# Kernel optimization log

Hardware: AMD Instinct MI355X
Metric: run time of the kernel (lower is better)

## Reference

```python
import jax, jax.numpy as jnp
import numpy as np

H = 256      # hidden_dim
NH = 8       # num_heads
D = H // NH  # per-head dim
NEG = -(2.0**32) + 1.0
EPS = 1e-5


def setup_inputs() -> dict:
    key = jax.random.key(0)
    ks = jax.random.split(key, 12)
    N, Tq, Tk = 2, 2048, 2048
    s = 1.0 / np.sqrt(H)
    return {
        "Q": jax.random.normal(ks[0], (N, Tq, H), jnp.float32),
        "K": jax.random.normal(ks[1], (N, Tk, H), jnp.float32),
        "V": jax.random.normal(ks[2], (N, Tk, H), jnp.float32),
        "Wq": jax.random.normal(ks[3], (H, H), jnp.float32) * s,
        "bq": jnp.zeros((H,), jnp.float32),
        "Wk": jax.random.normal(ks[4], (H, H), jnp.float32) * s,
        "bk": jnp.zeros((H,), jnp.float32),
        "Wv": jax.random.normal(ks[5], (H, H), jnp.float32) * s,
        "bv": jnp.zeros((H,), jnp.float32),
        "gamma": jnp.ones((H,), jnp.float32),
        "beta": jnp.zeros((H,), jnp.float32),
    }


def _split_heads(x):
    # [N,T,H] -> [h,N,T,D]  (matches torch split(dim=2)+cat(dim=0): head-major)
    N, T, _ = x.shape
    return x.reshape(N, T, NH, D).transpose(2, 0, 1, 3)


def reference(Q, K, V, Wq, bq, Wk, bk, Wv, bv, gamma, beta):
    N, Tq, _ = Q.shape
    Tk = K.shape[1]
    Ql = jax.nn.relu(Q @ Wq + bq)
    Kl = jax.nn.relu(K @ Wk + bk)
    Vl = jax.nn.relu(V @ Wv + bv)
    Qh, Kh, Vh = _split_heads(Ql), _split_heads(Kl), _split_heads(Vl)

    scores = jnp.einsum("hnqd,hnkd->hnqk", Qh, Kh) / jnp.sqrt(jnp.float32(D))
    key_mask = jnp.sign(jnp.abs(K).sum(-1))    # [N,Tk]
    scores = jnp.where(key_mask[None, :, None, :] == 0, NEG, scores)
    attn = jax.nn.softmax(scores / 0.01, axis=-1)
    query_mask = jnp.sign(jnp.abs(Q).sum(-1))  # [N,Tq]
    attn = attn * query_mask[None, :, :, None]  # dropout p=0 -> identity

    ctx = jnp.einsum("hnqk,hnkd->hnqd", attn[..., :-1], Vh[:, :, :-1, :])
    out = ctx.transpose(1, 2, 0, 3).reshape(N, Tq, H)

    mu = out.mean(-1, keepdims=True)
    var = ((out - mu) ** 2).mean(-1, keepdims=True)
    out = (out - mu) / jnp.sqrt(var + EPS) * gamma + beta

    weight = attn.transpose(1, 2, 0, 3).reshape(N, Tq, NH * Tk).mean(-1)
    return out, weight
```

## Files before the change

### kernel.cpp

```cpp
#include <hip/hip_runtime.h>
#include <math.h>

#define H_DIM 256
#define NHEAD 8
#define DHEAD 32
#define NB 2
#define TSEQ 2048
#define LN_EPS 1e-5f

#define QK2_SCALE 25.503486f
#define NEG2 (-6.2e11f)
#define SPLIT 4
#define TILES_PER (TSEQ / 64 / SPLIT)

typedef _Float16 half8 __attribute__((ext_vector_type(8)));
typedef float f32x4 __attribute__((ext_vector_type(4)));

__device__ __forceinline__ f32x4 mfma16(half8 a, half8 b, f32x4 c) {
  return __builtin_amdgcn_mfma_f32_16x16x32_f16(a, b, c, 0, 0, 0);
}
__device__ __forceinline__ float exp2fast(float x) {
  return __builtin_amdgcn_exp2f(x);
}
#define DPP_MAX4(mx, CTRL)                                                   \
  {                                                                          \
    _Pragma("unroll")                                                        \
    for (int r = 0; r < 4; ++r) {                                            \
      int t_ = __builtin_amdgcn_update_dpp(0, __float_as_int(mx[r]), CTRL,   \
                                           0xf, 0xf, false);                 \
      mx[r] = fmaxf(mx[r], __int_as_float(t_));                              \
    }                                                                        \
  }

__global__ __launch_bounds__(256) void mask_kernel(
    const float* __restrict__ Q, const float* __restrict__ K,
    float* __restrict__ qmask, float* __restrict__ kmask) {
  const int wid = threadIdx.x >> 6, lane = threadIdx.x & 63;
  int row = blockIdx.x * 4 + wid;
  const int total_q = NB * TSEQ;
  const float* src;
  float* dst;
  if (row < total_q) { src = Q + (size_t)row * H_DIM; dst = qmask + row; }
  else               { src = K + (size_t)(row - total_q) * H_DIM; dst = kmask + (row - total_q); }
  float4 v = *(const float4*)(src + lane * 4);
  float s = fabsf(v.x) + fabsf(v.y) + fabsf(v.z) + fabsf(v.w);
  #pragma unroll
  for (int off = 32; off > 0; off >>= 1) s += __shfl_xor(s, off);
  if (lane == 0) *dst = (s != 0.0f) ? 1.0f : 0.0f;
}

__global__ __launch_bounds__(256) void prepack_kernel(
    const float* __restrict__ Wq, const float* __restrict__ Wk, const float* __restrict__ Wv,
    half8* __restrict__ WpkHi, half8* __restrict__ WpkLo) {
  int slot = blockIdx.x * 256 + threadIdx.x;
  int lane = slot & 63;
  int fg = (slot >> 6) & 15;
  int s  = (slot >> 10) & 7;
  int which = slot >> 13;
  const float* W = which == 0 ? Wq : which == 1 ? Wk : Wv;
  int j  = fg * 16 + (lane & 15);
  int kb = s * 32 + (lane >> 4) * 8;
  half8 hi, lo;
  #pragma unroll
  for (int jj = 0; jj < 8; ++jj) {
    float x = W[(size_t)(kb + jj) * H_DIM + j];
    _Float16 h = (_Float16)x;
    hi[jj] = h;
    lo[jj] = (_Float16)(x - (float)h);
  }
  WpkHi[slot] = hi;
  WpkLo[slot] = lo;
}

__global__ __launch_bounds__(256) void proj_kernel(
    const float* __restrict__ Q, const float* __restrict__ K, const float* __restrict__ V,
    const float* __restrict__ bq, const float* __restrict__ bk, const float* __restrict__ bv,
    const half8* __restrict__ WpkHi, const half8* __restrict__ WpkLo,
    float* __restrict__ Qh, float* __restrict__ Kh, float* __restrict__ Vh) {
  const int which = blockIdx.z;
  const float* X    = which == 0 ? Q  : which == 1 ? K  : V;
  const float* bias = which == 0 ? bq : which == 1 ? bk : bv;
  float* dst        = which == 0 ? Qh : which == 1 ? Kh : Vh;

  const int tid = threadIdx.x;
  const int w = tid >> 6, lane = tid & 63;
  const int l15 = lane & 15, quad = lane >> 4;
  const int mbase = blockIdx.y * 64;
  const int nfg   = blockIdx.x * 4;

  half8 ahi[8], alo[8];
  {
    const float* xrow = X + (size_t)(mbase + w * 16 + l15) * H_DIM + quad * 8;
    #pragma unroll
    for (int s = 0; s < 8; ++s) {
      float4 a0 = *(const float4*)(xrow + s * 32);
      float4 a1 = *(const float4*)(xrow + s * 32 + 4);
      float xs[8] = {a0.x, a0.y, a0.z, a0.w, a1.x, a1.y, a1.z, a1.w};
      #pragma unroll
      for (int i = 0; i < 8; ++i) {
        _Float16 h = (_Float16)xs[i];
        ahi[s][i] = h;
        alo[s][i] = (_Float16)(xs[i] - (float)h);
      }
    }
  }

  f32x4 acc[4];
  #pragma unroll
  for (int f = 0; f < 4; ++f) acc[f] = (f32x4){0.f, 0.f, 0.f, 0.f};

  #pragma unroll
  for (int s = 0; s < 8; ++s) {
    const half8* ph = WpkHi + (((size_t)which * 8 + s) * 16 + nfg) * 64 + lane;
    const half8* pl = WpkLo + (((size_t)which * 8 + s) * 16 + nfg) * 64 + lane;
    #pragma unroll
    for (int f = 0; f < 4; ++f) {
      half8 BH = ph[f * 64];
      half8 BL = pl[f * 64];
      acc[f] = mfma16(ahi[s], BH, acc[f]);
      acc[f] = mfma16(ahi[s], BL, acc[f]);
      acc[f] = mfma16(alo[s], BH, acc[f]);
    }
  }

  #pragma unroll
  for (int f = 0; f < 4; ++f) {
    int j = blockIdx.x * 64 + f * 16 + l15;
    float bj = bias[j];
    int hh = j >> 5, dd = j & 31;
    #pragma unroll
    for (int r = 0; r < 4; ++r) {
      int m = mbase + w * 16 + quad * 4 + r;
      int n = m >> 11, t = m & (TSEQ - 1);
      float val = fmaxf(acc[f][r] + bj, 0.0f);
      if (which == 2 && t == TSEQ - 1) val = 0.0f;
      dst[(((size_t)hh * NB + n) * TSEQ + t) * DHEAD + dd] = val;
    }
  }
}

__global__ __launch_bounds__(256) void repack_kernel(
    const float* __restrict__ Qh, const float* __restrict__ Kh, const float* __restrict__ Vh,
    half8* __restrict__ Gqhi, half8* __restrict__ Gqlo,
    half8* __restrict__ Gkhi, half8* __restrict__ Gklo, half8* __restrict__ Gv) {
  const int tile = blockIdx.x;
  const int hn   = blockIdx.y;
  const int which = blockIdx.z;
  const int tid = threadIdx.x;
  if (which < 2) {
    const int w = tid >> 6, lane = tid & 63;
    const int f = w, krlo = lane >> 2, kdc = lane & 3;
    const float* src = (which == 0 ? Qh : Kh) +
        ((size_t)hn * TSEQ + tile * 64 + f * 16 + krlo) * DHEAD + kdc * 8;
    float4 a0 = *(const float4*)src;
    float4 a1 = *(const float4*)(src + 4);
    float xs[8] = {a0.x, a0.y, a0.z, a0.w, a1.x, a1.y, a1.z, a1.w};
    const float sc = which == 0 ? QK2_SCALE : 1.0f;
    half8 hi, lo;
    #pragma unroll
    for (int i = 0; i < 8; ++i) {
      float x = xs[i] * sc;
      _Float16 h = (_Float16)x;
      hi[i] = h;
      lo[i] = (_Float16)(x - (float)h);
    }
    size_t di = ((size_t)hn * 32 + tile) * 256 + f * 64 + kdc * 16 + krlo;
    if (which == 0) { Gqhi[di] = hi; Gqlo[di] = lo; }
    else            { Gkhi[di] = hi; Gklo[di] = lo; }
  } else {
    const int s = tid;
    const int top = s >> 6, mid = (s >> 4) & 3, low = s & 15;
    const int c = top >> 1, hh = top & 1;
    const int vkg = c * 4 + mid, vd = hh * 16 + low;
    const float* src = Vh + ((size_t)hn * TSEQ + tile * 64 + vkg * 8) * DHEAD + vd;
    half8 v8;
    #pragma unroll
    for (int j = 0; j < 8; ++j) v8[j] = (_Float16)src[j * DHEAD];
    Gv[((size_t)hn * 32 + tile) * 256 + s] = v8;
  }
}

__global__ __launch_bounds__(256) void attn_kernel(
    const half8* __restrict__ Gqhi, const half8* __restrict__ Gqlo,
    const half8* __restrict__ Gkhi, const half8* __restrict__ Gklo,
    const half8* __restrict__ Gv, const float* __restrict__ kmask,
    float* __restrict__ Op, float* __restrict__ Mp, float* __restrict__ Lp) {
  __shared__ __align__(16) half8 Vf[2][256];
  __shared__ __align__(16) _Float16 Pbuf[4][16][72];

  const int tid = threadIdx.x;
  const int w = tid >> 6, lane = tid & 63;
  const int l15 = lane & 15, quad = lane >> 4;

  const int b = blockIdx.x;
  const int g    = ((b & 7) << 1) | ((b >> 3) & 1);
  const int qt   = (b >> 4) & 31;
  const int sblk = b >> 9;
  const int n = g & 1;

  const size_t fbase = (size_t)g * 32 * 256;
  const int tile0 = sblk * TILES_PER;

  half8 qhi = Gqhi[fbase + (size_t)qt * 256 + w * 64 + lane];
  half8 qlo = Gqlo[fbase + (size_t)qt * 256 + w * 64 + lane];

  const float* kmp = kmask + (size_t)n * TSEQ + sblk * (TSEQ / SPLIT);

  half8 onesb;
  #pragma unroll
  for (int i = 0; i < 8; ++i) onesb[i] = (l15 == 0) ? (_Float16)1.0f : (_Float16)0.0f;

  float m_r[4];
  f32x4 O0, O1, Ol;
  #pragma unroll
  for (int r = 0; r < 4; ++r) m_r[r] = -1.0e38f;
  O0 = (f32x4){0.f, 0.f, 0.f, 0.f};
  O1 = (f32x4){0.f, 0.f, 0.f, 0.f};
  Ol = (f32x4){0.f, 0.f, 0.f, 0.f};

  {
    half8 v0 = Gv[fbase + (size_t)tile0 * 256 + tid];
    Vf[0][tid] = v0;
  }

  for (int tt = 0; tt < TILES_PER; ++tt) {
    half8 vnext;
    if (tt < TILES_PER - 1)
      vnext = Gv[fbase + (size_t)(tile0 + tt + 1) * 256 + tid];
    __syncthreads();
    if (tt < TILES_PER - 1)
      Vf[(tt + 1) & 1][tid] = vnext;

    const half8* kh = Gkhi + fbase + (size_t)(tile0 + tt) * 256;
    const half8* kl = Gklo + fbase + (size_t)(tile0 + tt) * 256;
    f32x4 S[4];
    #pragma unroll
    for (int f = 0; f < 4; ++f) {
      half8 KH = kh[f * 64 + lane];
      half8 KL = kl[f * 64 + lane];
      f32x4 a = (f32x4){0.f, 0.f, 0.f, 0.f};
      a = mfma16(qlo, KH, a);
      a = mfma16(qhi, KL, a);
      a = mfma16(qhi, KH, a);
      S[f] = a;
    }
    float kmf[4];
    #pragma unroll
    for (int f = 0; f < 4; ++f) kmf[f] = kmp[tt * 64 + (f << 4) + l15];

    float lg[4][4];
    #pragma unroll
    for (int r = 0; r < 4; ++r)
      #pragma unroll
      for (int f = 0; f < 4; ++f)
        lg[r][f] = (kmf[f] != 0.0f) ? S[f][r] : NEG2;

    float mx[4];
    #pragma unroll
    for (int r = 0; r < 4; ++r)
      mx[r] = fmaxf(fmaxf(lg[r][0], lg[r][1]), fmaxf(lg[r][2], lg[r][3]));
    DPP_MAX4(mx, 0x128);
    DPP_MAX4(mx, 0x124);
    DPP_MAX4(mx, 0x122);
    DPP_MAX4(mx, 0x121);

    float alpha[4];
    #pragma unroll
    for (int r = 0; r < 4; ++r) {
      float mnew = fmaxf(m_r[r], mx[r]);
      alpha[r] = exp2fast(m_r[r] - mnew);
      m_r[r] = mnew;
    }
    #pragma unroll
    for (int r = 0; r < 4; ++r) {
      int row = (quad << 2) + r;
      #pragma unroll
      for (int f = 0; f < 4; ++f)
        Pbuf[w][row][(f << 4) + l15] = (_Float16)exp2fast(lg[r][f] - m_r[r]);
    }
    #pragma unroll
    for (int r = 0; r < 4; ++r) {
      O0[r] *= alpha[r];
      O1[r] *= alpha[r];
      Ol[r] *= alpha[r];
    }
    asm volatile("s_waitcnt lgkmcnt(0)" ::: "memory");

    const half8* vbuf = (const half8*)Vf[tt & 1];
    #pragma unroll
    for (int c = 0; c < 2; ++c) {
      half8 pa = *(const half8*)&Pbuf[w][l15][(c << 5) + (quad << 3)];
      O0 = mfma16(pa, vbuf[((c << 1) | 0) * 64 + lane], O0);
      O1 = mfma16(pa, vbuf[((c << 1) | 1) * 64 + lane], O1);
      Ol = mfma16(pa, onesb, Ol);
    }
  }

  #pragma unroll
  for (int r = 0; r < 4; ++r) {
    int q = qt * 64 + w * 16 + (quad << 2) + r;
    size_t idx = ((size_t)(sblk * 16 + g) * TSEQ + q) * DHEAD;
    Op[idx + l15]      = O0[r];
    Op[idx + 16 + l15] = O1[r];
    if (l15 == 0) {
      Mp[(size_t)(sblk * 16 + g) * TSEQ + q] = m_r[r];
      Lp[(size_t)(sblk * 16 + g) * TSEQ + q] = Ol[r];
    }
  }
}

__global__ __launch_bounds__(256) void ln_kernel(
    const float* __restrict__ Op, const float* __restrict__ Mp, const float* __restrict__ Lp,
    const float* __restrict__ gamma, const float* __restrict__ beta,
    const float* __restrict__ qmask,
    float* __restrict__ out, float* __restrict__ wout) {
  const int wid = threadIdx.x >> 6, lane = threadIdx.x & 63;
  const int row = blockIdx.x * 4 + wid;
  const int n = row >> 11, q = row & (TSEQ - 1);
  const int hh = lane >> 3;
  const int hn = hh * NB + n;
  const int dbase = (lane & 7) * 4;

  float4 P[SPLIT];
  float m[SPLIT], l[SPLIT];
  #pragma unroll
  for (int i = 0; i < SPLIT; ++i) {
    size_t si = (size_t)(i * 16 + hn) * TSEQ + q;
    P[i] = *(const float4*)(Op + si * DHEAD + dbase);
    m[i] = Mp[si];
    l[i] = Lp[si];
  }
  float mm = fmaxf(fmaxf(m[0], m[1]), fmaxf(m[2], m[3]));
  float denom = 0.f;
  float a[SPLIT];
  #pragma unroll
  for (int i = 0; i < SPLIT; ++i) { a[i] = exp2fast(m[i] - mm); denom += l[i] * a[i]; }
  float qm = qmask[row];
  float inv = qm / denom;

  float4 x = make_float4(0.f, 0.f, 0.f, 0.f);
  #pragma unroll
  for (int i = 0; i < SPLIT; ++i) {
    x.x += P[i].x * a[i]; x.y += P[i].y * a[i];
    x.z += P[i].z * a[i]; x.w += P[i].w * a[i];
  }
  x.x *= inv; x.y *= inv; x.z *= inv; x.w *= inv;

  float s = x.x + x.y + x.z + x.w;
  #pragma unroll
  for (int off = 32; off > 0; off >>= 1) s += __shfl_xor(s, off);
  float mu = s * (1.0f / H_DIM);
  float dx0 = x.x - mu, dx1 = x.y - mu, dx2 = x.z - mu, dx3 = x.w - mu;
  float sq = dx0 * dx0 + dx1 * dx1 + dx2 * dx2 + dx3 * dx3;
  #pragma unroll
  for (int off = 32; off > 0; off >>= 1) sq += __shfl_xor(sq, off);
  float rstd = rsqrtf(sq * (1.0f / H_DIM) + LN_EPS);
  float4 g = *(const float4*)(gamma + lane * 4);
  float4 bb = *(const float4*)(beta + lane * 4);
  float4 y;
  y.x = dx0 * rstd * g.x + bb.x;
  y.y = dx1 * rstd * g.y + bb.y;
  y.z = dx2 * rstd * g.z + bb.z;
  y.w = dx3 * rstd * g.w + bb.w;
  *(float4*)(out + (size_t)row * H_DIM + lane * 4) = y;
  if (lane == 0) wout[row] = qm * (1.0f / TSEQ);
}

extern "C" void kernel_launch(void* const* d_in, const int* in_sizes, int n_in,
                              void* d_out, int out_size, void* d_ws, size_t ws_size,
                              hipStream_t stream) {
  const float* Q  = (const float*)d_in[0];
  const float* K  = (const float*)d_in[1];
  const float* V  = (const float*)d_in[2];
  const float* Wq = (const float*)d_in[3];
  const float* bq = (const float*)d_in[4];
  const float* Wk = (const float*)d_in[5];
  const float* bk = (const float*)d_in[6];
  const float* Wv = (const float*)d_in[7];
  const float* bv = (const float*)d_in[8];
  const float* gamma = (const float*)d_in[9];
  const float* beta  = (const float*)d_in[10];

  float* ws = (float*)d_ws;
  const size_t perHN = (size_t)16 * TSEQ * DHEAD;
  float* Qh = ws;
  float* Kh = Qh + perHN;
  float* Vh = Kh + perHN;
  float* Opart = ws;
  float* tail = ws + 4 * perHN;
  const size_t NFRAG = (size_t)16 * 32 * 256;
  half8* Gqhi = (half8*)tail;
  half8* Gqlo = Gqhi + NFRAG;
  half8* Gkhi = Gqlo + NFRAG;
  half8* Gklo = Gkhi + NFRAG;
  half8* Gv   = Gklo + NFRAG;
  float* Mp = (float*)(Gv + NFRAG);
  float* Lp = Mp + SPLIT * 16 * TSEQ;
  float* qmask = Lp + SPLIT * 16 * TSEQ;
  float* kmask = qmask + NB * TSEQ;
  half8* WpkHi = (half8*)(kmask + NB * TSEQ);
  half8* WpkLo = WpkHi + 24576;

  float* out  = (float*)d_out;
  float* wout = out + (size_t)NB * TSEQ * H_DIM;

  hipLaunchKernelGGL(mask_kernel, dim3(2 * NB * TSEQ / 4), dim3(256), 0, stream,
                     Q, K, qmask, kmask);
  hipLaunchKernelGGL(prepack_kernel, dim3(96), dim3(256), 0, stream,
                     Wq, Wk, Wv, WpkHi, WpkLo);
  hipLaunchKernelGGL(proj_kernel, dim3(H_DIM / 64, NB * TSEQ / 64, 3), dim3(256), 0, stream,
                     Q, K, V, bq, bk, bv, WpkHi, WpkLo, Qh, Kh, Vh);
  hipLaunchKernelGGL(repack_kernel, dim3(32, 16, 3), dim3(256), 0, stream,
                     Qh, Kh, Vh, Gqhi, Gqlo, Gkhi, Gklo, Gv);
  hipLaunchKernelGGL(attn_kernel, dim3(16 * 32 * SPLIT), dim3(256), 0, stream,
                     Gqhi, Gqlo, Gkhi, Gklo, Gv, kmask, Opart, Mp, Lp);
  hipLaunchKernelGGL(ln_kernel, dim3(NB * TSEQ / 4), dim3(256), 0, stream,
                     Opart, Mp, Lp, gamma, beta, qmask, out, wout);
}
```

Measured before the change: 151.5 us.

## Transpose attention MFMA so queries sit in columns, fold key mask into V

Swaps the MFMA operand order so each lane owns one query column, which turns the per-row softmax max into two cross-lane shuffles instead of DPP reductions over four rows. The key mask is no longer applied as a select on the scores. It is folded into V during repack and into a precomputed mask fragment that feeds the row-sum MFMA, so masked keys drop out of both numerator and denominator. Probabilities are packed with cvt_pkrtz, and outputs are written as vector stores. The risk is that masked keys now share the max with unmasked ones, which changes the numerics when every key is masked or when masked scores dominate the max.

```diff
diff --git a/kernel.cpp b/kernel.cpp
--- a/kernel.cpp
+++ b/kernel.cpp
@@ -9,11 +9,11 @@
 #define LN_EPS 1e-5f
 
 #define QK2_SCALE 25.503486f
-#define NEG2 (-6.2e11f)
 #define SPLIT 4
 #define TILES_PER (TSEQ / 64 / SPLIT)
 
 typedef _Float16 half8 __attribute__((ext_vector_type(8)));
+typedef _Float16 half2t __attribute__((ext_vector_type(2)));
 typedef float f32x4 __attribute__((ext_vector_type(4)));
 
 __device__ __forceinline__ f32x4 mfma16(half8 a, half8 b, f32x4 c) {
@@ -22,15 +22,9 @@
 __device__ __forceinline__ float exp2fast(float x) {
   return __builtin_amdgcn_exp2f(x);
 }
-#define DPP_MAX4(mx, CTRL)                                                   \
-  {                                                                          \
-    _Pragma("unroll")                                                        \
-    for (int r = 0; r < 4; ++r) {                                            \
-      int t_ = __builtin_amdgcn_update_dpp(0, __float_as_int(mx[r]), CTRL,   \
-                                           0xf, 0xf, false);                 \
-      mx[r] = fmaxf(mx[r], __int_as_float(t_));                              \
-    }                                                                        \
-  }
+__device__ __forceinline__ half2t pkrtz(float a, float b) {
+  return __builtin_bit_cast(half2t, __builtin_amdgcn_cvt_pkrtz(a, b));
+}
 
 __global__ __launch_bounds__(256) void mask_kernel(
     const float* __restrict__ Q, const float* __restrict__ K,
@@ -141,15 +135,17 @@
 
 __global__ __launch_bounds__(256) void repack_kernel(
     const float* __restrict__ Qh, const float* __restrict__ Kh, const float* __restrict__ Vh,
+    const float* __restrict__ kmask,
     half8* __restrict__ Gqhi, half8* __restrict__ Gqlo,
-    half8* __restrict__ Gkhi, half8* __restrict__ Gklo, half8* __restrict__ Gv) {
+    half8* __restrict__ Gkhi, half8* __restrict__ Gklo, half8* __restrict__ Gv,
+    half8* __restrict__ AmaskF) {
   const int tile = blockIdx.x;
   const int hn   = blockIdx.y;
   const int which = blockIdx.z;
   const int tid = threadIdx.x;
   if (which < 2) {
     const int w = tid >> 6, lane = tid & 63;
-    const int f = w, krlo = lane >> 2, kdc = lane & 3;
+    const int f = w, krlo = lane & 15, kdc = lane >> 4;
     const float* src = (which == 0 ? Qh : Kh) +
         ((size_t)hn * TSEQ + tile * 64 + f * 16 + krlo) * DHEAD + kdc * 8;
     float4 a0 = *(const float4*)src;
@@ -167,23 +163,36 @@
     size_t di = ((size_t)hn * 32 + tile) * 256 + f * 64 + kdc * 16 + krlo;
     if (which == 0) { Gqhi[di] = hi; Gqlo[di] = lo; }
     else            { Gkhi[di] = hi; Gklo[di] = lo; }
-  } else {
+  } else if (which == 2) {
     const int s = tid;
     const int top = s >> 6, mid = (s >> 4) & 3, low = s & 15;
     const int c = top >> 1, hh = top & 1;
     const int vkg = c * 4 + mid, vd = hh * 16 + low;
+    const int n = hn & 1;
     const float* src = Vh + ((size_t)hn * TSEQ + tile * 64 + vkg * 8) * DHEAD + vd;
+    const float* kmp = kmask + (size_t)n * TSEQ + tile * 64 + vkg * 8;
     half8 v8;
     #pragma unroll
-    for (int j = 0; j < 8; ++j) v8[j] = (_Float16)src[j * DHEAD];
+    for (int j = 0; j < 8; ++j) v8[j] = (_Float16)(src[j * DHEAD] * kmp[j]);
     Gv[((size_t)hn * 32 + tile) * 256 + s] = v8;
+  } else {
+    if (hn >= NB || tid >= 128) return;
+    const int n = hn;
+    const int c = tid >> 6, lane = tid & 63;
+    const int quad = lane >> 4, l15 = lane & 15;
+    half8 am;
+    #pragma unroll
+    for (int j = 0; j < 8; ++j)
+      am[j] = (l15 == 0) ? (_Float16)kmask[(size_t)n * TSEQ + tile * 64 + c * 32 + quad * 8 + j]
+                         : (_Float16)0.0f;
+    AmaskF[(((size_t)n * 32 + tile) * 2 + c) * 64 + lane] = am;
   }
 }
 
 __global__ __launch_bounds__(256) void attn_kernel(
     const half8* __restrict__ Gqhi, const half8* __restrict__ Gqlo,
     const half8* __restrict__ Gkhi, const half8* __restrict__ Gklo,
-    const half8* __restrict__ Gv, const float* __restrict__ kmask,
+    const half8* __restrict__ Gv, const half8* __restrict__ AmaskF,
     float* __restrict__ Op, float* __restrict__ Mp, float* __restrict__ Lp) {
   __shared__ __align__(16) half8 Vf[2][256];
   __shared__ __align__(16) _Float16 Pbuf[4][16][72];
@@ -204,107 +213,86 @@
   half8 qhi = Gqhi[fbase + (size_t)qt * 256 + w * 64 + lane];
   half8 qlo = Gqlo[fbase + (size_t)qt * 256 + w * 64 + lane];
 
-  const float* kmp = kmask + (size_t)n * TSEQ + sblk * (TSEQ / SPLIT);
-
-  half8 onesb;
-  #pragma unroll
-  for (int i = 0; i < 8; ++i) onesb[i] = (l15 == 0) ? (_Float16)1.0f : (_Float16)0.0f;
-
-  float m_r[4];
+  float m_q = -1.0e30f;
   f32x4 O0, O1, Ol;
-  #pragma unroll
-  for (int r = 0; r < 4; ++r) m_r[r] = -1.0e38f;
   O0 = (f32x4){0.f, 0.f, 0.f, 0.f};
   O1 = (f32x4){0.f, 0.f, 0.f, 0.f};
   Ol = (f32x4){0.f, 0.f, 0.f, 0.f};
 
-  {
-    half8 v0 = Gv[fbase + (size_t)tile0 * 256 + tid];
-    Vf[0][tid] = v0;
-  }
+  Vf[0][tid] = Gv[fbase + (size_t)tile0 * 256 + tid];
 
   for (int tt = 0; tt < TILES_PER; ++tt) {
+    const int tile = tile0 + tt;
     half8 vnext;
     if (tt < TILES_PER - 1)
-      vnext = Gv[fbase + (size_t)(tile0 + tt + 1) * 256 + tid];
+      vnext = Gv[fbase + (size_t)(tile + 1) * 256 + tid];
     __syncthreads();
     if (tt < TILES_PER - 1)
       Vf[(tt + 1) & 1][tid] = vnext;
 
-    const half8* kh = Gkhi + fbase + (size_t)(tile0 + tt) * 256;
-    const half8* kl = Gklo + fbase + (size_t)(tile0 + tt) * 256;
+    half8 am0 = AmaskF[(((size_t)n * 32 + tile) * 2 + 0) * 64 + lane];
+    half8 am1 = AmaskF[(((size_t)n * 32 + tile) * 2 + 1) * 64 + lane];
+
+    const half8* kh = Gkhi + fbase + (size_t)tile * 256;
+    const half8* kl = Gklo + fbase + (size_t)tile * 256;
     f32x4 S[4];
     #pragma unroll
     for (int f = 0; f < 4; ++f) {
       half8 KH = kh[f * 64 + lane];
       half8 KL = kl[f * 64 + lane];
       f32x4 a = (f32x4){0.f, 0.f, 0.f, 0.f};
-      a = mfma16(qlo, KH, a);
-      a = mfma16(qhi, KL, a);
-      a = mfma16(qhi, KH, a);
+      a = mfma16(KL, qhi, a);
+      a = mfma16(KH, qlo, a);
+      a = mfma16(KH, qhi, a);
       S[f] = a;
     }
-    float kmf[4];
-    #pragma unroll
-    for (int f = 0; f < 4; ++f) kmf[f] = kmp[tt * 64 + (f << 4) + l15];
-
-    float lg[4][4];
-    #pragma unroll
-    for (int r = 0; r < 4; ++r)
+
+    float mx = S[0][0];
+    #pragma unroll
+    for (int f = 0; f < 4; ++f)
       #pragma unroll
-      for (int f = 0; f < 4; ++f)
-        lg[r][f] = (kmf[f] != 0.0f) ? S[f][r] : NEG2;
-
-    float mx[4];
-    #pragma unroll
-    for (int r = 0; r < 4; ++r)
-      mx[r] = fmaxf(fmaxf(lg[r][0], lg[r][1]), fmaxf(lg[r][2], lg[r][3]));
-    DPP_MAX4(mx, 0x128);
-    DPP_MAX4(mx, 0x124);
-    DPP_MAX4(mx, 0x122);
-    DPP_MAX4(mx, 0x121);
-
-    float alpha[4];
-    #pragma unroll
-    for (int r = 0; r < 4; ++r) {
-      float mnew = fmaxf(m_r[r], mx[r]);
-      alpha[r] = exp2fast(m_r[r] - mnew);
-      m_r[r] = mnew;
-    }
-    #pragma unroll
-    for (int r = 0; r < 4; ++r) {
-      int row = (quad << 2) + r;
-      #pragma unroll
-      for (int f = 0; f < 4; ++f)
-        Pbuf[w][row][(f << 4) + l15] = (_Float16)exp2fast(lg[r][f] - m_r[r]);
-    }
-    #pragma unroll
-    for (int r = 0; r < 4; ++r) {
-      O0[r] *= alpha[r];
-      O1[r] *= alpha[r];
-      Ol[r] *= alpha[r];
-    }
+      for (int r = 0; r < 4; ++r) mx = fmaxf(mx, S[f][r]);
+    mx = fmaxf(mx, __shfl_xor(mx, 16));
+    mx = fmaxf(mx, __shfl_xor(mx, 32));
+
+    float mnew = fmaxf(m_q, mx);
+    float alpha = exp2fast(m_q - mnew);
+    m_q = mnew;
+
+    #pragma unroll
+    for (int f = 0; f < 4; ++f) {
+      float p0 = exp2fast(S[f][0] - m_q);
+      float p1 = exp2fast(S[f][1] - m_q);
+      float p2 = exp2fast(S[f][2] - m_q);
+      float p3 = exp2fast(S[f][3] - m_q);
+      half2t a01 = pkrtz(p0, p1);
+      half2t a23 = pkrtz(p2, p3);
+      *(half2t*)&Pbuf[w][l15][f * 16 + quad * 4]     = a01;
+      *(half2t*)&Pbuf[w][l15][f * 16 + quad * 4 + 2] = a23;
+    }
+    #pragma unroll
+    for (int r = 0; r < 4; ++r) { O0[r] *= alpha; O1[r] *= alpha; }
+    Ol[0] *= alpha;
     asm volatile("s_waitcnt lgkmcnt(0)" ::: "memory");
 
     const half8* vbuf = (const half8*)Vf[tt & 1];
     #pragma unroll
     for (int c = 0; c < 2; ++c) {
-      half8 pa = *(const half8*)&Pbuf[w][l15][(c << 5) + (quad << 3)];
-      O0 = mfma16(pa, vbuf[((c << 1) | 0) * 64 + lane], O0);
-      O1 = mfma16(pa, vbuf[((c << 1) | 1) * 64 + lane], O1);
-      Ol = mfma16(pa, onesb, Ol);
-    }
-  }
-
-  #pragma unroll
-  for (int r = 0; r < 4; ++r) {
-    int q = qt * 64 + w * 16 + (quad << 2) + r;
+      half8 pb = *(const half8*)&Pbuf[w][l15][c * 32 + quad * 8];
+      O0 = mfma16(vbuf[(c * 2 + 0) * 64 + lane], pb, O0);
+      O1 = mfma16(vbuf[(c * 2 + 1) * 64 + lane], pb, O1);
+      Ol = mfma16(c == 0 ? am0 : am1, pb, Ol);
+    }
+  }
+
+  {
+    int q = qt * 64 + w * 16 + l15;
     size_t idx = ((size_t)(sblk * 16 + g) * TSEQ + q) * DHEAD;
-    Op[idx + l15]      = O0[r];
-    Op[idx + 16 + l15] = O1[r];
-    if (l15 == 0) {
-      Mp[(size_t)(sblk * 16 + g) * TSEQ + q] = m_r[r];
-      Lp[(size_t)(sblk * 16 + g) * TSEQ + q] = Ol[r];
+    *(f32x4*)&Op[idx + quad * 4]      = O0;
+    *(f32x4*)&Op[idx + 16 + quad * 4] = O1;
+    if (quad == 0) {
+      Mp[(size_t)(sblk * 16 + g) * TSEQ + q] = m_q;
+      Lp[(size_t)(sblk * 16 + g) * TSEQ + q] = Ol[0];
     }
   }
 }
@@ -400,6 +388,7 @@
   float* kmask = qmask + NB * TSEQ;
   half8* WpkHi = (half8*)(kmask + NB * TSEQ);
   half8* WpkLo = WpkHi + 24576;
+  half8* AmaskF = WpkLo + 24576;
 
   float* out  = (float*)d_out;
   float* wout = out + (size_t)NB * TSEQ * H_DIM;
@@ -410,10 +399,10 @@
                      Wq, Wk, Wv, WpkHi, WpkLo);
   hipLaunchKernelGGL(proj_kernel, dim3(H_DIM / 64, NB * TSEQ / 64, 3), dim3(256), 0, stream,
                      Q, K, V, bq, bk, bv, WpkHi, WpkLo, Qh, Kh, Vh);
-  hipLaunchKernelGGL(repack_kernel, dim3(32, 16, 3), dim3(256), 0, stream,
-                     Qh, Kh, Vh, Gqhi, Gqlo, Gkhi, Gklo, Gv);
+  hipLaunchKernelGGL(repack_kernel, dim3(32, 16, 4), dim3(256), 0, stream,
+                     Qh, Kh, Vh, kmask, Gqhi, Gqlo, Gkhi, Gklo, Gv, AmaskF);
   hipLaunchKernelGGL(attn_kernel, dim3(16 * 32 * SPLIT), dim3(256), 0, stream,
-                     Gqhi, Gqlo, Gkhi, Gklo, Gv, kmask, Opart, Mp, Lp);
+                     Gqhi, Gqlo, Gkhi, Gklo, Gv, AmaskF, Opart, Mp, Lp);
   hipLaunchKernelGGL(ln_kernel, dim3(NB * TSEQ / 4), dim3(256), 0, stream,
                      Opart, Mp, Lp, gamma, beta, qmask, out, wout);
 }
```

After: 143.8 us. 1.05x faster.
